# Kernel optimization log

Measured on AMD Instinct MI355X. Metric: run time of the kernel, lower is better.

Reference implementation:

```python
import jax, jax.numpy as jnp
import numpy as np

N_NODES = 25000
N_EDGES = 400000
EMBED_DIM = 128
NUM_HEADS = 8
D_K = EMBED_DIM // NUM_HEADS


def setup_inputs() -> dict:
    key = jax.random.key(0)
    ks = jax.random.split(key, 8)
    sc = 1.0 / np.sqrt(EMBED_DIM)
    return {
        "x": jax.random.normal(ks[0], (N_NODES, EMBED_DIM), jnp.float32),
        "edge_index": jax.random.randint(ks[1], (2, N_EDGES), 0, N_NODES),
        "attn_bias": jax.random.normal(ks[2], (N_EDGES, NUM_HEADS), jnp.float32),
        "Wq": jax.random.normal(ks[3], (EMBED_DIM, EMBED_DIM), jnp.float32) * sc,
        "bq": jnp.zeros((EMBED_DIM,), jnp.float32),
        "Wk": jax.random.normal(ks[4], (EMBED_DIM, EMBED_DIM), jnp.float32) * sc,
        "bk": jnp.zeros((EMBED_DIM,), jnp.float32),
        "Wv": jax.random.normal(ks[5], (EMBED_DIM, EMBED_DIM), jnp.float32) * sc,
        "bv": jnp.zeros((EMBED_DIM,), jnp.float32),
        "Wo": jax.random.normal(ks[6], (EMBED_DIM, EMBED_DIM), jnp.float32) * sc,
        "bo": jnp.zeros((EMBED_DIM,), jnp.float32),
    }


def reference(x, edge_index, attn_bias, Wq, bq, Wk, bk, Wv, bv, Wo, bo):
    N = x.shape[0]
    E = edge_index.shape[1]
    H, dk = NUM_HEADS, D_K
    scale = 1.0 / np.sqrt(dk).astype(np.float32)
    dst = edge_index[0]  # query/aggregation node per edge
    src = edge_index[1]  # key/value node per edge

    # project at node level (as torch: linear(x)[index]), then gather per edge
    q = (x @ Wq.T + bq)[dst].reshape(E, H, dk)
    k = (x @ Wk.T + bk)[src].reshape(E, H, dk)
    v = (x @ Wv.T + bv)[src].reshape(E, H, dk)

    logits = scale * jnp.sum(q * k, axis=2) + attn_bias  # [E, H]

    # segment softmax over edges grouped by destination node
    m = jax.ops.segment_max(logits, dst, num_segments=N)     # [N, H]
    e = jnp.exp(logits - m[dst])                              # [E, H]
    z = jax.ops.segment_sum(e, dst, num_segments=N)           # [N, H]
    scores = e / z[dst]                                       # [E, H]

    agg = jax.ops.segment_sum(scores[..., None] * v, dst, num_segments=N)  # [N, H, dk]
    out = agg.reshape(N, H * dk) @ Wo.T + bo                   # [N, embed_dim]
    return out, logits[..., None]
```

## Files before the change

### kernel.cpp

```cpp
#include <hip/hip_runtime.h>
#include <math.h>

#define N_NODES 25000
#define N_EDGES 400000
#define EMBED   128
#define HEADS   8
#define DK      16
#define NBLK    98

typedef __attribute__((ext_vector_type(8))) short bf16x8;
typedef __attribute__((ext_vector_type(4))) float f32x4;
typedef unsigned int uint;
typedef unsigned short ushort;

__device__ inline uint pack2_bf16(float a, float b) {
    union { float f; uint u; } ua, ub;
    ua.f = a; ub.f = b;
    uint ra = (ua.u + 0x7FFFu + ((ua.u >> 16) & 1u)) >> 16;
    uint rb = (ub.u + 0x7FFFu + ((ub.u >> 16) & 1u)) >> 16;
    return (ra & 0xFFFFu) | (rb << 16);
}
__device__ inline ushort cvt_bf16(float a) {
    union { float f; uint u; } ua; ua.f = a;
    return (ushort)((ua.u + 0x7FFFu + ((ua.u >> 16) & 1u)) >> 16);
}
__device__ inline float bf16_lo(uint u) {
    union { uint u; float f; } x; x.u = u << 16; return x.f;
}
__device__ inline float bf16_hi(uint u) {
    union { uint u; float f; } x; x.u = u & 0xFFFF0000u; return x.f;
}

#define NX (N_NODES * 128)
__global__ __launch_bounds__(256) void convert_all(
    const float* __restrict__ x,
    const float* __restrict__ Wq, const float* __restrict__ Wk,
    const float* __restrict__ Wv, const float* __restrict__ Wo,
    ushort* __restrict__ xb, ushort* __restrict__ wb, int* __restrict__ deg)
{
    int i = blockIdx.x * 256 + threadIdx.x;
    if (i < N_NODES) deg[i] = 0;
    int base = i * 2;
    if (base < NX) {
        float2 v = *reinterpret_cast<const float2*>(x + base);
        reinterpret_cast<uint*>(xb)[i] = pack2_bf16(v.x, v.y);
    } else {
        int j = base - NX;
        if (j < 4 * 16384) {
            const float* src = (j < 16384) ? Wq + j
                             : (j < 32768) ? Wk + (j - 16384)
                             : (j < 49152) ? Wv + (j - 32768)
                             :               Wo + (j - 49152);
            float2 v = *reinterpret_cast<const float2*>(src);
            reinterpret_cast<uint*>(wb)[j >> 1] = pack2_bf16(v.x, v.y);
        }
    }
}

__global__ __launch_bounds__(256) void gemm_qkv_deg(
    const ushort* __restrict__ A, const ushort* __restrict__ Wall,
    const float* __restrict__ bq, const float* __restrict__ bk,
    const float* __restrict__ bv,
    ushort* __restrict__ Qb, ushort* __restrict__ Kb, ushort* __restrict__ Vb,
    const int* __restrict__ ei, int* __restrict__ deg,
    int M)
{
    const int which = blockIdx.y;
    if (which == 3) {
        int t = blockIdx.x * 256 + threadIdx.x;
        int e = t * 4;
        if (e + 3 < N_EDGES) {
            int4 d = *reinterpret_cast<const int4*>(ei + e);
            atomicAdd(&deg[d.x], 1);
            atomicAdd(&deg[d.y], 1);
            atomicAdd(&deg[d.z], 1);
            atomicAdd(&deg[d.w], 1);
        } else {
            for (; e < N_EDGES && e < t * 4 + 4; ++e)
                atomicAdd(&deg[ei[e]], 1);
        }
        return;
    }

    const ushort* W = Wall + which * 16384;
    const float* bias = (which == 0) ? bq : (which == 1) ? bk : bv;
    ushort* C = (which == 0) ? Qb : (which == 1) ? Kb : Vb;

    const int lane = threadIdx.x & 63;
    const int wave = threadIdx.x >> 6;
    const int ml   = lane & 15;
    const int quad = lane >> 4;
    const int m0   = blockIdx.x * 64 + wave * 16;

    int arow = m0 + ml; if (arow >= M) arow = M - 1;
    const ushort* ap = A + arow * 128 + quad * 8;

    f32x4 acc[8];
#pragma unroll
    for (int ct = 0; ct < 8; ++ct) acc[ct] = (f32x4){0.f, 0.f, 0.f, 0.f};

#pragma unroll
    for (int ks = 0; ks < 128; ks += 32) {
        bf16x8 af = *reinterpret_cast<const bf16x8*>(ap + ks);
#pragma unroll
        for (int ct = 0; ct < 8; ++ct) {
            bf16x8 bf = *reinterpret_cast<const bf16x8*>(
                W + (ct * 16 + ml) * 128 + ks + quad * 8);
            acc[ct] = __builtin_amdgcn_mfma_f32_16x16x32_bf16(af, bf, acc[ct], 0, 0, 0);
        }
    }

#pragma unroll
    for (int ct = 0; ct < 8; ++ct) {
        int col = ct * 16 + ml;
        float bv_ = bias[col];
#pragma unroll
        for (int r = 0; r < 4; ++r) {
            int row = m0 + quad * 4 + r;
            if (row < M)
                C[row * 128 + col] = cvt_bf16(acc[ct][r] + bv_);
        }
    }
}

__global__ __launch_bounds__(256) void gemm_out(
    const ushort* __restrict__ A, const ushort* __restrict__ W,
    const float* __restrict__ bias, float* __restrict__ C, int M)
{
    const int lane = threadIdx.x & 63;
    const int wave = threadIdx.x >> 6;
    const int ml   = lane & 15;
    const int quad = lane >> 4;
    const int m0   = blockIdx.x * 64 + wave * 16;

    int arow = m0 + ml; if (arow >= M) arow = M - 1;
    const ushort* ap = A + arow * 128 + quad * 8;

    f32x4 acc[8];
#pragma unroll
    for (int ct = 0; ct < 8; ++ct) acc[ct] = (f32x4){0.f, 0.f, 0.f, 0.f};

#pragma unroll
    for (int ks = 0; ks < 128; ks += 32) {
        bf16x8 af = *reinterpret_cast<const bf16x8*>(ap + ks);
#pragma unroll
        for (int ct = 0; ct < 8; ++ct) {
            bf16x8 bf = *reinterpret_cast<const bf16x8*>(
                W + (ct * 16 + ml) * 128 + ks + quad * 8);
            acc[ct] = __builtin_amdgcn_mfma_f32_16x16x32_bf16(af, bf, acc[ct], 0, 0, 0);
        }
    }

#pragma unroll
    for (int ct = 0; ct < 8; ++ct) {
        int col = ct * 16 + ml;
        float bv_ = bias[col];
#pragma unroll
        for (int r = 0; r < 4; ++r) {
            int row = m0 + quad * 4 + r;
            if (row < M)
                C[row * 128 + col] = acc[ct][r] + bv_;
        }
    }
}

__global__ __launch_bounds__(256) void scan_blocks(
    const int* __restrict__ deg, int* __restrict__ excl, int* __restrict__ bsum)
{
    __shared__ int sh[256];
    int t = threadIdx.x;
    int gid = blockIdx.x * 256 + t;
    int v = (gid < N_NODES) ? deg[gid] : 0;
    sh[t] = v;
    __syncthreads();
#pragma unroll
    for (int off = 1; off < 256; off <<= 1) {
        int u = (t >= off) ? sh[t - off] : 0;
        __syncthreads();
        sh[t] += u;
        __syncthreads();
    }
    if (gid < N_NODES) excl[gid] = sh[t] - v;
    if (t == 255) bsum[blockIdx.x] = sh[255];
}

__global__ __launch_bounds__(128) void scan_tops(
    const int* __restrict__ bsum, int* __restrict__ bbase)
{
    __shared__ int sh[128];
    int t = threadIdx.x;
    int v = (t < NBLK) ? bsum[t] : 0;
    sh[t] = v;
    __syncthreads();
#pragma unroll
    for (int off = 1; off < 128; off <<= 1) {
        int u = (t >= off) ? sh[t - off] : 0;
        __syncthreads();
        sh[t] += u;
        __syncthreads();
    }
    if (t < NBLK) bbase[t] = sh[t] - v;
}

__global__ __launch_bounds__(256) void scan_apply(
    int* __restrict__ excl, const int* __restrict__ bbase,
    int* __restrict__ cursor)
{
    int t = threadIdx.x;
    int gid = blockIdx.x * 256 + t;
    if (gid < N_NODES) {
        int o = excl[gid] + bbase[blockIdx.x];
        excl[gid] = o;
        cursor[gid] = o;
    }
    if (blockIdx.x == 0 && t == 0) excl[N_NODES] = N_EDGES;
}

__global__ __launch_bounds__(256) void scatter_edges(
    const int* __restrict__ ei, int* __restrict__ cursor,
    int2* __restrict__ csr2)
{
    int e = blockIdx.x * 256 + threadIdx.x;
    if (e >= N_EDGES) return;
    int dst = ei[e];
    int src = ei[N_EDGES + e];
    int pos = atomicAdd(&cursor[dst], 1);
    csr2[pos] = make_int2(e, src);
}

__global__ __launch_bounds__(256) void fused_attn(
    const ushort* __restrict__ Q2, const ushort* __restrict__ K2,
    const ushort* __restrict__ V2,
    const float* __restrict__ attn_bias,
    const int* __restrict__ offsets, const int2* __restrict__ csr2,
    float* __restrict__ logits, ushort* __restrict__ AGG)
{
    const int lane = threadIdx.x & 63;
    const int wid  = threadIdx.x >> 6;
    const int n = blockIdx.x * 4 + wid;
    const int start = offsets[n], end = offsets[n + 1];
    const int h  = lane & 7;
    const int es = lane >> 3;

    const uint4* Qu4 = reinterpret_cast<const uint4*>(Q2);
    const uint4* Ku4 = reinterpret_cast<const uint4*>(K2);
    const uint4* Vu4 = reinterpret_cast<const uint4*>(V2);

    uint4 qa = Qu4[n * 16 + h * 2];
    uint4 qb = Qu4[n * 16 + h * 2 + 1];
    float qf[16];
    {
        uint qq[8] = {qa.x, qa.y, qa.z, qa.w, qb.x, qb.y, qb.z, qb.w};
#pragma unroll
        for (int j = 0; j < 8; ++j) {
            qf[2 * j]     = bf16_lo(qq[j]);
            qf[2 * j + 1] = bf16_hi(qq[j]);
        }
    }

    float acc[16];
#pragma unroll
    for (int j = 0; j < 16; ++j) acc[j] = 0.f;
    float z = 0.f;

    for (int base = start; base < end; base += 8) {
        bool valid = (base + es) < end;
        int idx = base + es; if (!valid) idx = end - 1;
        int2 epair = csr2[idx];
        int e = epair.x, s = epair.y;

        uint4 k0 = Ku4[s * 16 + h * 2];
        uint4 k1 = Ku4[s * 16 + h * 2 + 1];
        uint4 v0 = Vu4[s * 16 + h * 2];
        uint4 v1 = Vu4[s * 16 + h * 2 + 1];
        float bias = attn_bias[e * 8 + h];

        uint kk[8] = {k0.x, k0.y, k0.z, k0.w, k1.x, k1.y, k1.z, k1.w};
        float d = 0.f;
#pragma unroll
        for (int j = 0; j < 8; ++j)
            d += qf[2 * j] * bf16_lo(kk[j]) + qf[2 * j + 1] * bf16_hi(kk[j]);

        float l = 0.25f * d + bias;
        float p = 0.f;
        if (valid) {
            logits[e * 8 + h] = l;
            p = __expf(l);
        }
        z += p;

        uint vv[8] = {v0.x, v0.y, v0.z, v0.w, v1.x, v1.y, v1.z, v1.w};
#pragma unroll
        for (int j = 0; j < 8; ++j) {
            acc[2 * j]     += p * bf16_lo(vv[j]);
            acc[2 * j + 1] += p * bf16_hi(vv[j]);
        }
    }

    {
        int bit = (lane >> 5) & 1;
#pragma unroll
        for (int j = 0; j < 8; ++j) {
            float send = bit ? acc[j] : acc[j + 8];
            float keep = bit ? acc[j + 8] : acc[j];
            acc[j] = keep + __shfl_xor(send, 32, 64);
        }
        bit = (lane >> 4) & 1;
#pragma unroll
        for (int j = 0; j < 4; ++j) {
            float send = bit ? acc[j] : acc[j + 4];
            float keep = bit ? acc[j + 4] : acc[j];
            acc[j] = keep + __shfl_xor(send, 16, 64);
        }
        bit = (lane >> 3) & 1;
#pragma unroll
        for (int j = 0; j < 2; ++j) {
            float send = bit ? acc[j] : acc[j + 2];
            float keep = bit ? acc[j + 2] : acc[j];
            acc[j] = keep + __shfl_xor(send, 8, 64);
        }
    }
    z += __shfl_xor(z, 8, 64);
    z += __shfl_xor(z, 16, 64);
    z += __shfl_xor(z, 32, 64);

    float inv = (z > 0.f) ? 1.f / z : 0.f;
    int d_off = ((lane >> 5) & 1) * 8 + ((lane >> 4) & 1) * 4 + ((lane >> 3) & 1) * 2;
    reinterpret_cast<uint*>(AGG)[n * 64 + h * 8 + (d_off >> 1)] =
        pack2_bf16(acc[0] * inv, acc[1] * inv);
}

extern "C" void kernel_launch(void* const* d_in, const int* in_sizes, int n_in,
                              void* d_out, int out_size, void* d_ws, size_t ws_size,
                              hipStream_t stream)
{
    const float* x         = (const float*)d_in[0];
    const int*   ei        = (const int*)  d_in[1];
    const float* attn_bias = (const float*)d_in[2];
    const float* Wq = (const float*)d_in[3];
    const float* bq = (const float*)d_in[4];
    const float* Wk = (const float*)d_in[5];
    const float* bk = (const float*)d_in[6];
    const float* Wv = (const float*)d_in[7];
    const float* bv = (const float*)d_in[8];
    const float* Wo = (const float*)d_in[9];
    const float* bo = (const float*)d_in[10];

    float* out    = (float*)d_out;
    float* logits = out + N_NODES * EMBED;

    ushort* xb   = (ushort*)d_ws;
    ushort* wb   = xb + NX;
    ushort* Qb   = wb + 4 * 16384;
    ushort* Kb   = Qb + NX;
    ushort* Vb   = Kb + NX;
    ushort* AGGb = Vb + NX;
    int* deg     = (int*)(AGGb + NX);
    int* offsets = deg + N_NODES;
    int* cursor  = offsets + N_NODES + 1;
    int2* csr2   = (int2*)(cursor + N_NODES);
    int* bsum    = (int*)(csr2 + N_EDGES);
    int* bbase   = bsum + NBLK;

    int npairs = (NX + 4 * 16384) / 2;
    convert_all<<<(npairs + 255) / 256, 256, 0, stream>>>(x, Wq, Wk, Wv, Wo, xb, wb, deg);

    int gblocks = (N_NODES + 63) / 64;
    dim3 qkvgrid(gblocks, 4);
    gemm_qkv_deg<<<qkvgrid, 256, 0, stream>>>(xb, wb, bq, bk, bv, Qb, Kb, Vb,
                                              ei, deg, N_NODES);

    scan_blocks<<<NBLK, 256, 0, stream>>>(deg, offsets, bsum);
    scan_tops<<<1, 128, 0, stream>>>(bsum, bbase);
    scan_apply<<<NBLK, 256, 0, stream>>>(offsets, bbase, cursor);
    scatter_edges<<<(N_EDGES + 255) / 256, 256, 0, stream>>>(ei, cursor, csr2);

    fused_attn<<<N_NODES / 4, 256, 0, stream>>>(Qb, Kb, Vb, attn_bias,
                                                offsets, csr2, logits, AGGb);

    gemm_out<<<gblocks, 256, 0, stream>>>(AGGb, wb + 3 * 16384, bo, out, N_NODES);
}
```

Before: 210.1 us.

## Fuse x conversion into QKV GEMM, drop scan_tops, unroll attention edge loop

The separate fp32-to-bf16 pass over x is removed. The QKV GEMM now reads fp32 x directly and packs it to bf16 in registers, which saves a full write and re-read of the converted activations but triples the redundant x loads across the three projections. The single-block scan_tops kernel is removed; each scan_apply block computes its own prefix base by summing earlier block sums with a wave reduction. The attention loop now handles two edges per lane per iteration, giving more memory-level parallelism for the K/V gathers.

```diff
diff --git a/kernel.cpp b/kernel.cpp
--- a/kernel.cpp
+++ b/kernel.cpp
@@ -32,33 +32,26 @@
 }
 
 #define NX (N_NODES * 128)
-__global__ __launch_bounds__(256) void convert_all(
-    const float* __restrict__ x,
+__global__ __launch_bounds__(256) void convert_w_deg(
     const float* __restrict__ Wq, const float* __restrict__ Wk,
     const float* __restrict__ Wv, const float* __restrict__ Wo,
-    ushort* __restrict__ xb, ushort* __restrict__ wb, int* __restrict__ deg)
+    ushort* __restrict__ wb, int* __restrict__ deg)
 {
     int i = blockIdx.x * 256 + threadIdx.x;
     if (i < N_NODES) deg[i] = 0;
-    int base = i * 2;
-    if (base < NX) {
-        float2 v = *reinterpret_cast<const float2*>(x + base);
-        reinterpret_cast<uint*>(xb)[i] = pack2_bf16(v.x, v.y);
-    } else {
-        int j = base - NX;
-        if (j < 4 * 16384) {
-            const float* src = (j < 16384) ? Wq + j
-                             : (j < 32768) ? Wk + (j - 16384)
-                             : (j < 49152) ? Wv + (j - 32768)
-                             :               Wo + (j - 49152);
-            float2 v = *reinterpret_cast<const float2*>(src);
-            reinterpret_cast<uint*>(wb)[j >> 1] = pack2_bf16(v.x, v.y);
-        }
+    if (i < 32768) {
+        int j = i * 2;
+        const float* src = (j < 16384) ? Wq + j
+                         : (j < 32768) ? Wk + (j - 16384)
+                         : (j < 49152) ? Wv + (j - 32768)
+                         :               Wo + (j - 49152);
+        float2 v = *reinterpret_cast<const float2*>(src);
+        reinterpret_cast<uint*>(wb)[i] = pack2_bf16(v.x, v.y);
     }
 }
 
 __global__ __launch_bounds__(256) void gemm_qkv_deg(
-    const ushort* __restrict__ A, const ushort* __restrict__ Wall,
+    const float* __restrict__ x, const ushort* __restrict__ Wall,
     const float* __restrict__ bq, const float* __restrict__ bk,
     const float* __restrict__ bv,
     ushort* __restrict__ Qb, ushort* __restrict__ Kb, ushort* __restrict__ Vb,
@@ -93,7 +86,7 @@
     const int m0   = blockIdx.x * 64 + wave * 16;
 
     int arow = m0 + ml; if (arow >= M) arow = M - 1;
-    const ushort* ap = A + arow * 128 + quad * 8;
+    const float4* xf4 = reinterpret_cast<const float4*>(x) + arow * 32 + quad * 2;
 
     f32x4 acc[8];
 #pragma unroll
@@ -101,7 +94,16 @@
 
 #pragma unroll
     for (int ks = 0; ks < 128; ks += 32) {
-        bf16x8 af = *reinterpret_cast<const bf16x8*>(ap + ks);
+        float4 f0 = xf4[ks >> 2];
+        float4 f1 = xf4[(ks >> 2) + 1];
+        bf16x8 af;
+        {
+            uint* au = reinterpret_cast<uint*>(&af);
+            au[0] = pack2_bf16(f0.x, f0.y);
+            au[1] = pack2_bf16(f0.z, f0.w);
+            au[2] = pack2_bf16(f1.x, f1.y);
+            au[3] = pack2_bf16(f1.z, f1.w);
+        }
 #pragma unroll
         for (int ct = 0; ct < 8; ++ct) {
             bf16x8 bf = *reinterpret_cast<const bf16x8*>(
@@ -184,32 +186,23 @@
     if (t == 255) bsum[blockIdx.x] = sh[255];
 }
 
-__global__ __launch_bounds__(128) void scan_tops(
-    const int* __restrict__ bsum, int* __restrict__ bbase)
-{
-    __shared__ int sh[128];
+__global__ __launch_bounds__(256) void scan_apply(
+    int* __restrict__ excl, const int* __restrict__ bsum,
+    int* __restrict__ cursor)
+{
+    __shared__ int base_sh;
     int t = threadIdx.x;
-    int v = (t < NBLK) ? bsum[t] : 0;
-    sh[t] = v;
+    if (t < 64) {
+        int s = 0;
+        for (int i = t; i < (int)blockIdx.x; i += 64) s += bsum[i];
+#pragma unroll
+        for (int off = 32; off; off >>= 1) s += __shfl_xor(s, off, 64);
+        if (t == 0) base_sh = s;
+    }
     __syncthreads();
-#pragma unroll
-    for (int off = 1; off < 128; off <<= 1) {
-        int u = (t >= off) ? sh[t - off] : 0;
-        __syncthreads();
-        sh[t] += u;
-        __syncthreads();
-    }
-    if (t < NBLK) bbase[t] = sh[t] - v;
-}
-
-__global__ __launch_bounds__(256) void scan_apply(
-    int* __restrict__ excl, const int* __restrict__ bbase,
-    int* __restrict__ cursor)
-{
-    int t = threadIdx.x;
     int gid = blockIdx.x * 256 + t;
     if (gid < N_NODES) {
-        int o = excl[gid] + bbase[blockIdx.x];
+        int o = excl[gid] + base_sh;
         excl[gid] = o;
         cursor[gid] = o;
     }
@@ -228,6 +221,19 @@
     csr2[pos] = make_int2(e, src);
 }
 
+__device__ inline float dot16(const float* qf, uint4 a, uint4 b) {
+    float d = 0.f;
+    d += qf[0]  * bf16_lo(a.x) + qf[1]  * bf16_hi(a.x);
+    d += qf[2]  * bf16_lo(a.y) + qf[3]  * bf16_hi(a.y);
+    d += qf[4]  * bf16_lo(a.z) + qf[5]  * bf16_hi(a.z);
+    d += qf[6]  * bf16_lo(a.w) + qf[7]  * bf16_hi(a.w);
+    d += qf[8]  * bf16_lo(b.x) + qf[9]  * bf16_hi(b.x);
+    d += qf[10] * bf16_lo(b.y) + qf[11] * bf16_hi(b.y);
+    d += qf[12] * bf16_lo(b.z) + qf[13] * bf16_hi(b.z);
+    d += qf[14] * bf16_lo(b.w) + qf[15] * bf16_hi(b.w);
+    return d;
+}
+
 __global__ __launch_bounds__(256) void fused_attn(
     const ushort* __restrict__ Q2, const ushort* __restrict__ K2,
     const ushort* __restrict__ V2,
@@ -263,37 +269,35 @@
     for (int j = 0; j < 16; ++j) acc[j] = 0.f;
     float z = 0.f;
 
-    for (int base = start; base < end; base += 8) {
-        bool valid = (base + es) < end;
-        int idx = base + es; if (!valid) idx = end - 1;
-        int2 epair = csr2[idx];
-        int e = epair.x, s = epair.y;
-
-        uint4 k0 = Ku4[s * 16 + h * 2];
-        uint4 k1 = Ku4[s * 16 + h * 2 + 1];
-        uint4 v0 = Vu4[s * 16 + h * 2];
-        uint4 v1 = Vu4[s * 16 + h * 2 + 1];
-        float bias = attn_bias[e * 8 + h];
-
-        uint kk[8] = {k0.x, k0.y, k0.z, k0.w, k1.x, k1.y, k1.z, k1.w};
-        float d = 0.f;
-#pragma unroll
-        for (int j = 0; j < 8; ++j)
-            d += qf[2 * j] * bf16_lo(kk[j]) + qf[2 * j + 1] * bf16_hi(kk[j]);
-
-        float l = 0.25f * d + bias;
-        float p = 0.f;
-        if (valid) {
-            logits[e * 8 + h] = l;
-            p = __expf(l);
-        }
-        z += p;
-
-        uint vv[8] = {v0.x, v0.y, v0.z, v0.w, v1.x, v1.y, v1.z, v1.w};
+    for (int base = start; base < end; base += 16) {
+        int i0 = base + es;     bool ok0 = i0 < end; if (!ok0) i0 = start;
+        int i1 = base + 8 + es; bool ok1 = i1 < end; if (!ok1) i1 = start;
+        int2 p0 = csr2[i0];
+        int2 p1 = csr2[i1];
+
+        uint4 k00 = Ku4[p0.y * 16 + h * 2], k01 = Ku4[p0.y * 16 + h * 2 + 1];
+        uint4 k10 = Ku4[p1.y * 16 + h * 2], k11 = Ku4[p1.y * 16 + h * 2 + 1];
+        uint4 v00 = Vu4[p0.y * 16 + h * 2], v01 = Vu4[p0.y * 16 + h * 2 + 1];
+        uint4 v10 = Vu4[p1.y * 16 + h * 2], v11 = Vu4[p1.y * 16 + h * 2 + 1];
+        float b0 = attn_bias[p0.x * 8 + h];
+        float b1 = attn_bias[p1.x * 8 + h];
+
+        float d0 = dot16(qf, k00, k01);
+        float d1 = dot16(qf, k10, k11);
+        float l0 = 0.25f * d0 + b0;
+        float l1 = 0.25f * d1 + b1;
+
+        float pe0 = 0.f, pe1 = 0.f;
+        if (ok0) { logits[p0.x * 8 + h] = l0; pe0 = __expf(l0); }
+        if (ok1) { logits[p1.x * 8 + h] = l1; pe1 = __expf(l1); }
+        z += pe0 + pe1;
+
+        uint w0[8] = {v00.x, v00.y, v00.z, v00.w, v01.x, v01.y, v01.z, v01.w};
+        uint w1[8] = {v10.x, v10.y, v10.z, v10.w, v11.x, v11.y, v11.z, v11.w};
 #pragma unroll
         for (int j = 0; j < 8; ++j) {
-            acc[2 * j]     += p * bf16_lo(vv[j]);
-            acc[2 * j + 1] += p * bf16_hi(vv[j]);
+            acc[2 * j]     += pe0 * bf16_lo(w0[j]) + pe1 * bf16_lo(w1[j]);
+            acc[2 * j + 1] += pe0 * bf16_hi(w0[j]) + pe1 * bf16_hi(w1[j]);
         }
     }
 
@@ -349,8 +353,7 @@
     float* out    = (float*)d_out;
     float* logits = out + N_NODES * EMBED;
 
-    ushort* xb   = (ushort*)d_ws;
-    ushort* wb   = xb + NX;
+    ushort* wb   = (ushort*)d_ws;
     ushort* Qb   = wb + 4 * 16384;
     ushort* Kb   = Qb + NX;
     ushort* Vb   = Kb + NX;
@@ -360,19 +363,16 @@
     int* cursor  = offsets + N_NODES + 1;
     int2* csr2   = (int2*)(cursor + N_NODES);
     int* bsum    = (int*)(csr2 + N_EDGES);
-    int* bbase   = bsum + NBLK;
-
-    int npairs = (NX + 4 * 16384) / 2;
-    convert_all<<<(npairs + 255) / 256, 256, 0, stream>>>(x, Wq, Wk, Wv, Wo, xb, wb, deg);
+
+    convert_w_deg<<<128, 256, 0, stream>>>(Wq, Wk, Wv, Wo, wb, deg);
 
     int gblocks = (N_NODES + 63) / 64;
     dim3 qkvgrid(gblocks, 4);
-    gemm_qkv_deg<<<qkvgrid, 256, 0, stream>>>(xb, wb, bq, bk, bv, Qb, Kb, Vb,
+    gemm_qkv_deg<<<qkvgrid, 256, 0, stream>>>(x, wb, bq, bk, bv, Qb, Kb, Vb,
                                               ei, deg, N_NODES);
 
     scan_blocks<<<NBLK, 256, 0, stream>>>(deg, offsets, bsum);
-    scan_tops<<<1, 128, 0, stream>>>(bsum, bbase);
-    scan_apply<<<NBLK, 256, 0, stream>>>(offsets, bbase, cursor);
+    scan_apply<<<NBLK, 256, 0, stream>>>(offsets, bsum, cursor);
     scatter_edges<<<(N_EDGES + 255) / 256, 256, 0, stream>>>(ei, cursor, csr2);
 
     fused_attn<<<N_NODES / 4, 256, 0, stream>>>(Qb, Kb, Vb, attn_bias,
```

Result: slower. 221.3 us (+5.3%).
